# Performance work log

Hardware: AMD Instinct MI355X
Metric: run time of the kernel (lower is better)

The kernel has to match this reference:

```python
import jax, jax.numpy as jnp
import numpy as np

HEADS = 8

def setup_inputs() -> dict:
    key = jax.random.key(0)
    ks = jax.random.split(key, 4)
    b, n, d = 4, 4097, 128  # n = 64*64 + 1 (CLS + spatial)
    x = jax.random.normal(ks[0], (b, n, d), dtype=jnp.float32)
    W_qkv = jax.random.normal(ks[1], (d, 3 * d), dtype=jnp.float32) * (d ** -0.5)
    b_qkv = jnp.zeros((3 * d,), dtype=jnp.float32)
    W_out = jax.random.normal(ks[2], (d, d), dtype=jnp.float32) * (d ** -0.5)
    b_out = jnp.zeros((d,), dtype=jnp.float32)
    return {"x": x, "W_qkv": W_qkv, "b_qkv": b_qkv, "W_out": W_out, "b_out": b_out}

def reference(x, W_qkv, b_qkv, W_out, b_out):
    b, n, d = x.shape
    h = HEADS
    dh = d // h
    scale = d ** -0.5  # note: module scales by dim**-0.5, not head_dim**-0.5
    qkv = x @ W_qkv + b_qkv                      # [b, n, 3d]
    q, k, v = jnp.split(qkv, 3, axis=-1)
    def to_heads(t):
        return t.reshape(b, n, h, dh).transpose(0, 2, 1, 3)  # [b, h, n, dh]
    q, k, v = to_heads(q), to_heads(k), to_heads(v)
    dots = jnp.einsum('bhid,bhjd->bhij', q, k) * scale       # [b, h, n, n]
    attn = jax.nn.softmax(dots, axis=-1)
    out = jnp.einsum('bhij,bhjd->bhid', attn, v)             # [b, h, n, dh]
    out = out.transpose(0, 2, 1, 3).reshape(b, n, d)
    return out @ W_out + b_out
```

## Files before the change

### kernel.cpp

```cpp
#include <hip/hip_runtime.h>
#include <hip/hip_bf16.h>
#include <stdint.h>


#define BB 4
#define NN 4097
#define NNP 4112
#define DD 128
#define HH 8
#define DH 16
#define BH (BB*HH)
#define ROWS (BB*NN)
#define MT  1025
#define NSP 4

typedef _Float16 h4 __attribute__((ext_vector_type(4)));
typedef _Float16 h8 __attribute__((ext_vector_type(8)));
typedef __fp16   fp16v2 __attribute__((ext_vector_type(2)));
typedef float    f4 __attribute__((ext_vector_type(4)));

#define QSCALE (0.08838834764831845f * 1.4426950408889634f)

#if __has_builtin(__builtin_amdgcn_exp2f)
#define EXP2F(x) __builtin_amdgcn_exp2f(x)
#else
#define EXP2F(x) exp2f(x)
#endif

union H4u { h4 v; fp16v2 p[2]; };
union H8u { h8 v; fp16v2 p[4]; };

static __device__ __forceinline__ H4u pack4u(float a, float b, float c, float d) {
    H4u u;
#if __has_builtin(__builtin_amdgcn_cvt_pkrtz)
    u.p[0] = __builtin_amdgcn_cvt_pkrtz(a, b);
    u.p[1] = __builtin_amdgcn_cvt_pkrtz(c, d);
#else
    u.v[0] = (_Float16)a; u.v[1] = (_Float16)b; u.v[2] = (_Float16)c; u.v[3] = (_Float16)d;
#endif
    return u;
}

static __device__ __forceinline__ h8 pack8u(const float4& t0, const float4& t1) {
    H8u u;
#if __has_builtin(__builtin_amdgcn_cvt_pkrtz)
    u.p[0] = __builtin_amdgcn_cvt_pkrtz(t0.x, t0.y);
    u.p[1] = __builtin_amdgcn_cvt_pkrtz(t0.z, t0.w);
    u.p[2] = __builtin_amdgcn_cvt_pkrtz(t1.x, t1.y);
    u.p[3] = __builtin_amdgcn_cvt_pkrtz(t1.z, t1.w);
#else
    u.v[0]=(_Float16)t0.x; u.v[1]=(_Float16)t0.y; u.v[2]=(_Float16)t0.z; u.v[3]=(_Float16)t0.w;
    u.v[4]=(_Float16)t1.x; u.v[5]=(_Float16)t1.y; u.v[6]=(_Float16)t1.z; u.v[7]=(_Float16)t1.w;
#endif
    return u.v;
}

__global__ __launch_bounds__(256) void prep(
    const float* __restrict__ Wqkv,
    const float* __restrict__ Wout,
    _Float16* __restrict__ WqkvT,
    _Float16* __restrict__ WoutT)
{
    const int id = blockIdx.x*256 + threadIdx.x;
    if (id < 384*128) {
        const int n = id >> 7, k = id & 127;
        const float s = (n < 128) ? QSCALE : 1.0f;
        WqkvT[id] = (_Float16)(Wqkv[k*384 + n] * s);
    } else if (id < 384*128 + 128*128) {
        const int e = id - 384*128;
        const int n = e >> 7, k = e & 127;
        WoutT[e] = (_Float16)(Wout[k*128 + n]);
    }
}

__global__ __launch_bounds__(256) void qkv_mfma(
    const float* __restrict__ x,
    const _Float16* __restrict__ WqkvT,
    const float* __restrict__ bqkv,
    _Float16* __restrict__ Qh,
    _Float16* __restrict__ Kh,
    _Float16* __restrict__ Vt)
{
    __shared__ _Float16 tile[16][264];
    const int wid  = blockIdx.x;
    const int wave = threadIdx.x >> 6;
    const int lane = threadIdx.x & 63;
    const int quad = lane >> 4, l16 = lane & 15;

    const int rowlo = wid*16;
    const int blo   = rowlo / NN;
    const bool vfast = (rowlo + 15 < ROWS) && (rowlo + 15 - blo*NN < NN);
    const int nrow0 = rowlo - blo*NN;

    const int arow = rowlo + l16;
    const int arc  = (arow < ROWS) ? arow : (ROWS - 1);
    const float* xr = x + (size_t)arc*DD;
    h8 af[4];
    #pragma unroll
    for (int kk = 0; kk < 4; ++kk) {
        const float4 t0 = *(const float4*)(xr + kk*32 + quad*8);
        const float4 t1 = *(const float4*)(xr + kk*32 + quad*8 + 4);
        af[kk] = pack8u(t0, t1);
    }

    const int nt0 = wave*6;

    for (int nt = nt0; nt < nt0 + 6; nt += 2) {
        const float b0 = bqkv[nt*16 + l16]      * ((nt   < 8) ? QSCALE : 1.0f);
        const float b1 = bqkv[nt*16 + 16 + l16] * ((nt+1 < 8) ? QSCALE : 1.0f);
        f4 a0 = {b0,b0,b0,b0}, a1 = {b1,b1,b1,b1};
        #pragma unroll
        for (int kk = 0; kk < 4; ++kk) {
            const h8 bf0 = *(const h8*)(WqkvT + (size_t)(nt*16      + l16)*DD + kk*32 + quad*8);
            const h8 bf1 = *(const h8*)(WqkvT + (size_t)(nt*16 + 16 + l16)*DD + kk*32 + quad*8);
            a0 = __builtin_amdgcn_mfma_f32_16x16x32_f16(af[kk], bf0, a0, 0, 0, 0);
            a1 = __builtin_amdgcn_mfma_f32_16x16x32_f16(af[kk], bf1, a1, 0, 0, 0);
        }
        #pragma unroll
        for (int u = 0; u < 2; ++u) {
            const int ntc = nt + u;
            const f4 av = u ? a1 : a0;
            if (ntc < 16) {
                #pragma unroll
                for (int r = 0; r < 4; ++r)
                    tile[quad*4 + r][ntc*16 + l16] = (_Float16)av[r];
            } else {
                const int head = ntc & 7;
                if (vfast) {
                    h4 pk;
                    pk[0] = (_Float16)av[0]; pk[1] = (_Float16)av[1];
                    pk[2] = (_Float16)av[2]; pk[3] = (_Float16)av[3];
                    *(h4*)(Vt + ((size_t)(blo*HH + head)*DH + l16)*NNP + nrow0 + quad*4) = pk;
                } else {
                    #pragma unroll
                    for (int r = 0; r < 4; ++r) {
                        const int row = rowlo + quad*4 + r;
                        if (row < ROWS) {
                            const int bidx = row / NN;
                            const int nrow = row - bidx*NN;
                            Vt[((size_t)(bidx*HH + head)*DH + l16)*NNP + nrow] = (_Float16)av[r];
                        }
                    }
                }
            }
        }
    }
    __syncthreads();

    {
        const int u   = threadIdx.x;
        const int ntc = u >> 4, lt = u & 15;
        const int row = rowlo + lt;
        if (row < ROWS) {
            _Float16* base = (ntc < 8) ? Qh : Kh;
            const int head = ntc & 7;
            const int bidx = row / NN;
            const int nrow = row - bidx*NN;
            _Float16* dst = base + ((size_t)(bidx*HH + head)*NNP + nrow)*DH;
            *(h8*)dst       = *(const h8*)&tile[lt][ntc*16];
            *(h8*)(dst + 8) = *(const h8*)&tile[lt][ntc*16 + 8];
        }
    }
}

__global__ __launch_bounds__(256, 8) void attn_mfma(
    const _Float16* __restrict__ Qh,
    const _Float16* __restrict__ Kh,
    const _Float16* __restrict__ Vt,
    _Float16* __restrict__ PACC,
    float* __restrict__ PL)
{
    const int qt   = blockIdx.x;
    const int bh   = blockIdx.y;
    const int sp   = blockIdx.z;
    const int tid  = threadIdx.x;
    const int wave = tid >> 6;
    const int lane = tid & 63;
    const int quad = lane >> 4;
    const int l16  = lane & 15;
    const int bidx = bh >> 3, head = bh & 7;

    const int qbase = qt*256 + wave*64;

    const _Float16* Qb = Qh + (size_t)bh*NNP*DH;
    h4 qf[4];
    #pragma unroll
    for (int g = 0; g < 4; ++g) {
        const int qr = qbase + g*16 + l16;
        const int qc = (qr < NN) ? qr : (NN-1);
        qf[g] = *(const h4*)(Qb + (size_t)qc*DH + quad*4);
    }

    f4 acc[4] = {{0,0,0,0},{0,0,0,0},{0,0,0,0},{0,0,0,0}};
    float ls[4] = {0.f,0.f,0.f,0.f};

    const int t0 = sp*64;
    const int t1 = t0 + 64;

    const _Float16* kp = Kh + ((size_t)bh*NNP + (size_t)t0*16 + l16)*DH + quad*4;
    const _Float16* vp = Vt + ((size_t)bh*DH + l16)*NNP + t0*16 + quad*4;

    h4 ak = *(const h4*)kp;
    h4 av = *(const h4*)vp;
    const f4 zero = {0.f,0.f,0.f,0.f};
#if __has_builtin(__builtin_amdgcn_fdot2)
    const fp16v2 one2 = {(__fp16)1.0f, (__fp16)1.0f};
#endif

    for (int tt = t0; tt < t1; ++tt) {
        kp += 16*DH; vp += 16;
        const h4 nak = *(const h4*)kp;
        const h4 nav = *(const h4*)vp;
        #pragma unroll
        for (int g = 0; g < 4; ++g) {
            f4 d = __builtin_amdgcn_mfma_f32_16x16x16f16(ak, qf[g], zero, 0, 0, 0);
            const float p0 = EXP2F(d[0]), p1 = EXP2F(d[1]), p2 = EXP2F(d[2]), p3 = EXP2F(d[3]);
            const H4u pb = pack4u(p0, p1, p2, p3);
#if __has_builtin(__builtin_amdgcn_fdot2)
            ls[g] = __builtin_amdgcn_fdot2(pb.p[0], one2,
                     __builtin_amdgcn_fdot2(pb.p[1], one2, ls[g], false), false);
#else
            ls[g] += (p0 + p1) + (p2 + p3);
#endif
            acc[g] = __builtin_amdgcn_mfma_f32_16x16x16f16(av, pb.v, acc[g], 0, 0, 0);
        }
        ak = nak; av = nav;
    }

    if (sp == 3) {
        #pragma unroll
        for (int g = 0; g < 4; ++g) {
            f4 d = __builtin_amdgcn_mfma_f32_16x16x16f16(ak, qf[g], zero, 0, 0, 0);
            const float p0 = (quad == 0) ? EXP2F(d[0]) : 0.f;
            ls[g] += p0;
            const H4u pb = pack4u(p0, 0.f, 0.f, 0.f);
            acc[g] = __builtin_amdgcn_mfma_f32_16x16x16f16(av, pb.v, acc[g], 0, 0, 0);
        }
    }

    #pragma unroll
    for (int g = 0; g < 4; ++g) {
        float l = ls[g];
        l += __shfl_xor(l, 16);
        l += __shfl_xor(l, 32);
        const int qr = qbase + g*16 + l16;
        if (qr < NN) {
            const size_t row = (size_t)bidx*NN + qr;
            const float inv = 1.0f / l;
            const H4u st = pack4u(acc[g][0]*inv, acc[g][1]*inv, acc[g][2]*inv, acc[g][3]*inv);
            *(h4*)(PACC + (row*NSP + sp)*DD + head*DH + quad*4) = st.v;
            if (quad == 0) PL[(row*HH + head)*NSP + sp] = l;
        }
    }
}

__global__ __launch_bounds__(256) void out_mfma(
    const _Float16* __restrict__ PACC,
    const float* __restrict__ PL,
    const _Float16* __restrict__ WoutT,
    const float* __restrict__ bout,
    float* __restrict__ out)
{
    __shared__ _Float16 afl[16][136];
    const int wid  = blockIdx.x;
    const int tid  = threadIdx.x;
    const int wave = tid >> 6;
    const int lane = tid & 63;
    const int quad = lane >> 4, l16 = lane & 15;
    const int nt   = wave*2;

    h8 wf[2][4];
    #pragma unroll
    for (int u = 0; u < 2; ++u)
        #pragma unroll
        for (int kk = 0; kk < 4; ++kk)
            wf[u][kk] = *(const h8*)(WoutT + (size_t)((nt+u)*16 + l16)*DD + kk*32 + quad*8);
    const float b0 = bout[nt*16 + l16];
    const float b1 = bout[nt*16 + 16 + l16];

    {
        const int t   = tid >> 4;
        const int seg = tid & 15;
        const int head = seg >> 1;
        const int arow = wid*16 + t;
        const int arc  = (arow < ROWS) ? arow : (ROWS - 1);
        const f4 lv = *(const f4*)(PL + ((size_t)arc*HH + head)*NSP);
        const float lsum = (lv[0] + lv[1]) + (lv[2] + lv[3]);
        const float inv = 1.0f / lsum;
        const _Float16* pb = PACC + (size_t)arc*NSP*DD + seg*8;
        float m[8] = {0,0,0,0,0,0,0,0};
        #pragma unroll
        for (int sp = 0; sp < NSP; ++sp) {
            const float s = lv[sp]*inv;
            const h8 p = *(const h8*)(pb + sp*DD);
            #pragma unroll
            for (int j = 0; j < 8; ++j) m[j] += s*(float)p[j];
        }
        H8u u;
#if __has_builtin(__builtin_amdgcn_cvt_pkrtz)
        u.p[0] = __builtin_amdgcn_cvt_pkrtz(m[0], m[1]);
        u.p[1] = __builtin_amdgcn_cvt_pkrtz(m[2], m[3]);
        u.p[2] = __builtin_amdgcn_cvt_pkrtz(m[4], m[5]);
        u.p[3] = __builtin_amdgcn_cvt_pkrtz(m[6], m[7]);
#else
        #pragma unroll
        for (int j = 0; j < 8; ++j) u.v[j] = (_Float16)m[j];
#endif
        *(h8*)&afl[t][seg*8] = u.v;
    }
    __syncthreads();

    h8 af[4];
    #pragma unroll
    for (int kk = 0; kk < 4; ++kk)
        af[kk] = *(const h8*)&afl[l16][kk*32 + quad*8];

    f4 a0 = {b0,b0,b0,b0}, a1 = {b1,b1,b1,b1};
    #pragma unroll
    for (int kk = 0; kk < 4; ++kk) {
        a0 = __builtin_amdgcn_mfma_f32_16x16x32_f16(af[kk], wf[0][kk], a0, 0, 0, 0);
        a1 = __builtin_amdgcn_mfma_f32_16x16x32_f16(af[kk], wf[1][kk], a1, 0, 0, 0);
    }
    const int r0 = wid*16 + quad*4;
    #pragma unroll
    for (int r = 0; r < 4; ++r) {
        const int row = r0 + r;
        if (row < ROWS) {
            out[(size_t)row*DD + nt*16      + l16] = a0[r];
            out[(size_t)row*DD + nt*16 + 16 + l16] = a1[r];
        }
    }
}

extern "C" void kernel_launch(void* const* d_in, const int* in_sizes, int n_in,
                              void* d_out, int out_size, void* d_ws, size_t ws_size,
                              hipStream_t stream) {
    const float* x    = (const float*)d_in[0];
    const float* Wqkv = (const float*)d_in[1];
    const float* bqkv = (const float*)d_in[2];
    const float* Wout = (const float*)d_in[3];
    const float* bout = (const float*)d_in[4];
    for (int i = 0; i < n_in; ++i) {
        switch (in_sizes[i]) {
            case 2097664: x    = (const float*)d_in[i]; break;
            case 49152:   Wqkv = (const float*)d_in[i]; break;
            case 384:     bqkv = (const float*)d_in[i]; break;
            case 16384:   Wout = (const float*)d_in[i]; break;
            case 128:     bout = (const float*)d_in[i]; break;
            default: break;
        }
    }
    float* out = (float*)d_out;

    const size_t perh = (size_t)BH * NNP * DH;
    _Float16* Qh   = (_Float16*)d_ws;
    _Float16* Kh   = Qh + perh;
    _Float16* Vt   = Kh + perh;
    _Float16* PACC = Vt + perh;
    float*    PL    = (float*)(PACC + (size_t)NSP*ROWS*DD);
    _Float16* WqkvT = (_Float16*)(PL + (size_t)NSP*ROWS*HH);
    _Float16* WoutT = WqkvT + 384*128;

    const int prep_total = 384*128 + 128*128;

    hipLaunchKernelGGL(prep, dim3((prep_total + 255)/256), dim3(256), 0, stream,
                       Wqkv, Wout, WqkvT, WoutT);
    hipLaunchKernelGGL(qkv_mfma, dim3(MT), dim3(256), 0, stream,
                       x, WqkvT, bqkv, Qh, Kh, Vt);
    hipLaunchKernelGGL(attn_mfma, dim3(17, BH, NSP), dim3(256), 0, stream,
                       Qh, Kh, Vt, PACC, PL);
    hipLaunchKernelGGL(out_mfma, dim3(MT), dim3(256), 0, stream,
                       PACC, PL, WoutT, bout, out);
}
```

Baseline: 175.8 us.

## Widen QKV and output projection blocks to 512 threads, redistributing tiles

The QKV projection kernel now uses 8 waves per block, each computing 3 output column tiles instead of 6, which gives more wave-level parallelism per 16-row tile. The output projection kernel now handles 32 rows per 512-thread block, with two row groups of four waves each. It also loads Wout fragments inside the MFMA loop instead of preloading them. The aim is to raise occupancy and latency hiding in these two smaller kernels. The cost is more redundant x and Wout loads per block and larger shared tiles.

```diff
diff --git a/kernel.cpp b/kernel.cpp
--- a/kernel.cpp
+++ b/kernel.cpp
@@ -73,7 +73,7 @@
     }
 }
 
-__global__ __launch_bounds__(256) void qkv_mfma(
+__global__ __launch_bounds__(512) void qkv_mfma(
     const float* __restrict__ x,
     const _Float16* __restrict__ WqkvT,
     const float* __restrict__ bqkv,
@@ -103,43 +103,35 @@
         af[kk] = pack8u(t0, t1);
     }
 
-    const int nt0 = wave*6;
-
-    for (int nt = nt0; nt < nt0 + 6; nt += 2) {
-        const float b0 = bqkv[nt*16 + l16]      * ((nt   < 8) ? QSCALE : 1.0f);
-        const float b1 = bqkv[nt*16 + 16 + l16] * ((nt+1 < 8) ? QSCALE : 1.0f);
-        f4 a0 = {b0,b0,b0,b0}, a1 = {b1,b1,b1,b1};
+    #pragma unroll
+    for (int i = 0; i < 3; ++i) {
+        const int ntc = wave + 8*i;
+        const float b0 = bqkv[ntc*16 + l16] * ((ntc < 8) ? QSCALE : 1.0f);
+        f4 a0 = {b0,b0,b0,b0};
         #pragma unroll
         for (int kk = 0; kk < 4; ++kk) {
-            const h8 bf0 = *(const h8*)(WqkvT + (size_t)(nt*16      + l16)*DD + kk*32 + quad*8);
-            const h8 bf1 = *(const h8*)(WqkvT + (size_t)(nt*16 + 16 + l16)*DD + kk*32 + quad*8);
+            const h8 bf0 = *(const h8*)(WqkvT + (size_t)(ntc*16 + l16)*DD + kk*32 + quad*8);
             a0 = __builtin_amdgcn_mfma_f32_16x16x32_f16(af[kk], bf0, a0, 0, 0, 0);
-            a1 = __builtin_amdgcn_mfma_f32_16x16x32_f16(af[kk], bf1, a1, 0, 0, 0);
-        }
-        #pragma unroll
-        for (int u = 0; u < 2; ++u) {
-            const int ntc = nt + u;
-            const f4 av = u ? a1 : a0;
-            if (ntc < 16) {
+        }
+        if (ntc < 16) {
+            #pragma unroll
+            for (int r = 0; r < 4; ++r)
+                tile[quad*4 + r][ntc*16 + l16] = (_Float16)a0[r];
+        } else {
+            const int head = ntc & 7;
+            if (vfast) {
+                h4 pk;
+                pk[0] = (_Float16)a0[0]; pk[1] = (_Float16)a0[1];
+                pk[2] = (_Float16)a0[2]; pk[3] = (_Float16)a0[3];
+                *(h4*)(Vt + ((size_t)(blo*HH + head)*DH + l16)*NNP + nrow0 + quad*4) = pk;
+            } else {
                 #pragma unroll
-                for (int r = 0; r < 4; ++r)
-                    tile[quad*4 + r][ntc*16 + l16] = (_Float16)av[r];
-            } else {
-                const int head = ntc & 7;
-                if (vfast) {
-                    h4 pk;
-                    pk[0] = (_Float16)av[0]; pk[1] = (_Float16)av[1];
-                    pk[2] = (_Float16)av[2]; pk[3] = (_Float16)av[3];
-                    *(h4*)(Vt + ((size_t)(blo*HH + head)*DH + l16)*NNP + nrow0 + quad*4) = pk;
-                } else {
-                    #pragma unroll
-                    for (int r = 0; r < 4; ++r) {
-                        const int row = rowlo + quad*4 + r;
-                        if (row < ROWS) {
-                            const int bidx = row / NN;
-                            const int nrow = row - bidx*NN;
-                            Vt[((size_t)(bidx*HH + head)*DH + l16)*NNP + nrow] = (_Float16)av[r];
-                        }
+                for (int r = 0; r < 4; ++r) {
+                    const int row = rowlo + quad*4 + r;
+                    if (row < ROWS) {
+                        const int bidx = row / NN;
+                        const int nrow = row - bidx*NN;
+                        Vt[((size_t)(bidx*HH + head)*DH + l16)*NNP + nrow] = (_Float16)a0[r];
                     }
                 }
             }
@@ -147,11 +139,11 @@
     }
     __syncthreads();
 
-    {
+    if (threadIdx.x < 384) {
         const int u   = threadIdx.x;
         const int ntc = u >> 4, lt = u & 15;
         const int row = rowlo + lt;
-        if (row < ROWS) {
+        if (ntc < 16 && row < ROWS) {
             _Float16* base = (ntc < 8) ? Qh : Kh;
             const int head = ntc & 7;
             const int bidx = row / NN;
@@ -254,35 +246,24 @@
     }
 }
 
-__global__ __launch_bounds__(256) void out_mfma(
+__global__ __launch_bounds__(512) void out_mfma(
     const _Float16* __restrict__ PACC,
     const float* __restrict__ PL,
     const _Float16* __restrict__ WoutT,
     const float* __restrict__ bout,
     float* __restrict__ out)
 {
-    __shared__ _Float16 afl[16][136];
-    const int wid  = blockIdx.x;
+    __shared__ _Float16 afl[32][136];
     const int tid  = threadIdx.x;
     const int wave = tid >> 6;
     const int lane = tid & 63;
     const int quad = lane >> 4, l16 = lane & 15;
-    const int nt   = wave*2;
-
-    h8 wf[2][4];
-    #pragma unroll
-    for (int u = 0; u < 2; ++u)
-        #pragma unroll
-        for (int kk = 0; kk < 4; ++kk)
-            wf[u][kk] = *(const h8*)(WoutT + (size_t)((nt+u)*16 + l16)*DD + kk*32 + quad*8);
-    const float b0 = bout[nt*16 + l16];
-    const float b1 = bout[nt*16 + 16 + l16];
 
     {
-        const int t   = tid >> 4;
+        const int t2  = tid >> 4;
         const int seg = tid & 15;
         const int head = seg >> 1;
-        const int arow = wid*16 + t;
+        const int arow = blockIdx.x*32 + t2;
         const int arc  = (arow < ROWS) ? arow : (ROWS - 1);
         const f4 lv = *(const f4*)(PL + ((size_t)arc*HH + head)*NSP);
         const float lsum = (lv[0] + lv[1]) + (lv[2] + lv[3]);
@@ -306,20 +287,28 @@
         #pragma unroll
         for (int j = 0; j < 8; ++j) u.v[j] = (_Float16)m[j];
 #endif
-        *(h8*)&afl[t][seg*8] = u.v;
+        *(h8*)&afl[t2][seg*8] = u.v;
     }
     __syncthreads();
 
+    const int tw  = wave >> 2;
+    const int nt  = (wave & 3)*2;
+    const int wid = blockIdx.x*2 + tw;
+
     h8 af[4];
     #pragma unroll
     for (int kk = 0; kk < 4; ++kk)
-        af[kk] = *(const h8*)&afl[l16][kk*32 + quad*8];
-
+        af[kk] = *(const h8*)&afl[tw*16 + l16][kk*32 + quad*8];
+
+    const float b0 = bout[nt*16 + l16];
+    const float b1 = bout[nt*16 + 16 + l16];
     f4 a0 = {b0,b0,b0,b0}, a1 = {b1,b1,b1,b1};
     #pragma unroll
     for (int kk = 0; kk < 4; ++kk) {
-        a0 = __builtin_amdgcn_mfma_f32_16x16x32_f16(af[kk], wf[0][kk], a0, 0, 0, 0);
-        a1 = __builtin_amdgcn_mfma_f32_16x16x32_f16(af[kk], wf[1][kk], a1, 0, 0, 0);
+        const h8 wf0 = *(const h8*)(WoutT + (size_t)(nt*16      + l16)*DD + kk*32 + quad*8);
+        const h8 wf1 = *(const h8*)(WoutT + (size_t)(nt*16 + 16 + l16)*DD + kk*32 + quad*8);
+        a0 = __builtin_amdgcn_mfma_f32_16x16x32_f16(af[kk], wf0, a0, 0, 0, 0);
+        a1 = __builtin_amdgcn_mfma_f32_16x16x32_f16(af[kk], wf1, a1, 0, 0, 0);
     }
     const int r0 = wid*16 + quad*4;
     #pragma unroll
@@ -365,10 +354,10 @@
 
     hipLaunchKernelGGL(prep, dim3((prep_total + 255)/256), dim3(256), 0, stream,
                        Wqkv, Wout, WqkvT, WoutT);
-    hipLaunchKernelGGL(qkv_mfma, dim3(MT), dim3(256), 0, stream,
+    hipLaunchKernelGGL(qkv_mfma, dim3(MT), dim3(512), 0, stream,
                        x, WqkvT, bqkv, Qh, Kh, Vt);
     hipLaunchKernelGGL(attn_mfma, dim3(17, BH, NSP), dim3(256), 0, stream,
                        Qh, Kh, Vt, PACC, PL);
-    hipLaunchKernelGGL(out_mfma, dim3(MT), dim3(256), 0, stream,
+    hipLaunchKernelGGL(out_mfma, dim3((MT + 1)/2), dim3(512), 0, stream,
                        PACC, PL, WoutT, bout, out);
 }
```

New measurement: 178.7 us. Within noise of the previous version (+1.6%).
